# Kernel optimization log

Hardware: AMD Instinct MI355X
Metric: run time of the kernel (lower is better)

## Reference

```python
import jax, jax.numpy as jnp
import numpy as np

EPS = 1e-5  # eps placed on the diagonal via the 'eye' buffer in the torch module


def setup_inputs() -> dict:
    key = jax.random.key(0)
    k1, k2, k3 = jax.random.split(key, 3)
    B, C, H, W = 32, 256, 64, 64
    F = C // 4
    x = jax.random.normal(k1, (B, C, H, W), dtype=jnp.float32)
    # affine mixing weight [4,4,F] (torch inits diag(0.5,1,1,1); we add noise to exercise all paths)
    weight = jnp.eye(4, dtype=jnp.float32)[:, :, None] * jnp.ones((F,), jnp.float32) \
             + 0.1 * jax.random.normal(k2, (4, 4, F), dtype=jnp.float32)
    bias = 0.1 * jax.random.normal(k3, (4, F), dtype=jnp.float32)
    return {"x": x, "weight": weight, "bias": bias}


def reference(x, weight, bias):
    B, C, H, W = x.shape
    F = C // 4
    # split channels into 4 quaternion components: [4, B, F, H, W]
    xq = x.reshape(B, 4, F, H, W).transpose(1, 0, 2, 3, 4)
    # per (component, channel) mean over batch+spatial
    mean = xq.mean(axis=(1, 3, 4))                       # [4, F]
    xc = xq - mean[:, None, :, None, None]               # centered
    N = B * H * W
    # covariance across the 4 quaternion components, per channel: [F, 4, 4]
    v = xc.transpose(2, 0, 1, 3, 4).reshape(F, 4, N)     # [F, 4, N]
    cov = jnp.einsum('fin,fjn->fij', v, v) / N
    # batched 4x4 Cholesky and lower-triangular whitening solve
    L = jnp.linalg.cholesky(cov + EPS * jnp.eye(4, dtype=x.dtype))  # [F, 4, 4]
    z = jax.scipy.linalg.solve_triangular(L, v, lower=True)         # [F, 4, N]
    z = z.reshape(F, 4, B, H, W).transpose(1, 2, 0, 3, 4)           # [4, B, F, H, W]
    # unrolled 4x4 affine mix + bias, per channel
    out = jnp.einsum('ijf,jbfhw->ibfhw', weight, z) + bias[:, None, :, None, None]
    # re-concatenate components along channels -> [B, C, H, W]
    return out.transpose(1, 0, 2, 3, 4).reshape(B, C, H, W)
```

## Files before the change

### kernel.cpp

```cpp
#include <hip/hip_runtime.h>
#include <math.h>

constexpr int B   = 32;
constexpr int C   = 256;
constexpr int F   = 64;
constexpr int HW  = 64 * 64;
constexpr int HW4 = HW / 4;
constexpr int P4  = B * HW4;
constexpr float EPSV = 1e-5f;

constexpr int SBLOCKS = 32;
constexpr int SITER   = P4 / (SBLOCKS * 256);
constexpr int TBLOCKS = P4 / 256;

__global__ __launch_bounds__(256) void stats_kernel(const float* __restrict__ x,
                                                    float* __restrict__ sums) {
    const int f     = blockIdx.x / SBLOCKS;
    const int chunk = blockIdx.x % SBLOCKS;
    const int tid   = threadIdx.x;

    float acc[14];
#pragma unroll
    for (int i = 0; i < 14; ++i) acc[i] = 0.f;

    const float4* xb = reinterpret_cast<const float4*>(x);

#pragma unroll
    for (int it = 0; it < SITER; ++it) {
        const int p   = chunk * (256 * SITER) + it * 256 + tid;
        const int b   = p >> 10;
        const int hw4 = p & (HW4 - 1);
        float4 v[4];
#pragma unroll
        for (int q = 0; q < 4; ++q)
            v[q] = xb[(size_t)(b * C + q * F + f) * HW4 + hw4];
#pragma unroll
        for (int l = 0; l < 4; ++l) {
            float e0 = ((const float*)&v[0])[l];
            float e1 = ((const float*)&v[1])[l];
            float e2 = ((const float*)&v[2])[l];
            float e3 = ((const float*)&v[3])[l];
            acc[0] += e0; acc[1] += e1; acc[2] += e2; acc[3] += e3;
            acc[4]  += e0 * e0; acc[5]  += e0 * e1; acc[6]  += e0 * e2; acc[7]  += e0 * e3;
            acc[8]  += e1 * e1; acc[9]  += e1 * e2; acc[10] += e1 * e3;
            acc[11] += e2 * e2; acc[12] += e2 * e3;
            acc[13] += e3 * e3;
        }
    }

#pragma unroll
    for (int i = 0; i < 14; ++i) {
#pragma unroll
        for (int off = 32; off >= 1; off >>= 1)
            acc[i] += __shfl_down(acc[i], off, 64);
    }

    __shared__ float red[4][14];
    const int wave = tid >> 6;
    const int lane = tid & 63;
    if (lane == 0) {
#pragma unroll
        for (int i = 0; i < 14; ++i) red[wave][i] = acc[i];
    }
    __syncthreads();
    if (tid < 14) {
        float t = red[0][tid] + red[1][tid] + red[2][tid] + red[3][tid];
        atomicAdd(&sums[f * 14 + tid], t);
    }
}

__global__ __launch_bounds__(64) void solve_kernel(const float* __restrict__ sums,
                                                   const float* __restrict__ weight,
                                                   const float* __restrict__ bias,
                                                   float* __restrict__ Mc) {
    const int f = threadIdx.x;
    if (f >= F) return;
    const float invN = 1.0f / (float)(B * HW);

    float m[4];
#pragma unroll
    for (int q = 0; q < 4; ++q) m[q] = sums[f * 14 + q] * invN;

    float cov[4][4];
    {
        int k = 4;
        for (int i = 0; i < 4; ++i)
            for (int j = i; j < 4; ++j) {
                float cij = sums[f * 14 + k] * invN - m[i] * m[j];
                cov[i][j] = cij;
                cov[j][i] = cij;
                ++k;
            }
    }
#pragma unroll
    for (int i = 0; i < 4; ++i) cov[i][i] += EPSV;

    float L[4][4] = {};
    for (int i = 0; i < 4; ++i) {
        for (int j = 0; j <= i; ++j) {
            float s = cov[i][j];
            for (int k = 0; k < j; ++k) s -= L[i][k] * L[j][k];
            if (i == j) L[i][j] = sqrtf(s);
            else        L[i][j] = s / L[j][j];
        }
    }
    float Li[4][4] = {};
    for (int j = 0; j < 4; ++j) {
        Li[j][j] = 1.0f / L[j][j];
        for (int i = j + 1; i < 4; ++i) {
            float s = 0.f;
            for (int k = j; k < i; ++k) s += L[i][k] * Li[k][j];
            Li[i][j] = -s / L[i][i];
        }
    }
    float M[4][4];
    for (int i = 0; i < 4; ++i)
        for (int j = 0; j < 4; ++j) {
            float s = 0.f;
            for (int k = 0; k < 4; ++k)
                s += weight[(i * 4 + k) * F + f] * Li[k][j];
            M[i][j] = s;
        }
    for (int i = 0; i < 4; ++i) {
        float ci = bias[i * F + f];
        for (int j = 0; j < 4; ++j) ci -= M[i][j] * m[j];
#pragma unroll
        for (int j = 0; j < 4; ++j) Mc[f * 20 + i * 4 + j] = M[i][j];
        Mc[f * 20 + 16 + i] = ci;
    }
}

__global__ __launch_bounds__(256) void transform_kernel(const float* __restrict__ x,
                                                        const float* __restrict__ Mc,
                                                        float* __restrict__ out) {
    const int f     = blockIdx.x / TBLOCKS;
    const int chunk = blockIdx.x % TBLOCKS;

    __shared__ float sM[20];
    if (threadIdx.x < 20) sM[threadIdx.x] = Mc[f * 20 + threadIdx.x];
    __syncthreads();

    const int p   = chunk * 256 + threadIdx.x;
    const int b   = p >> 10;
    const int hw4 = p & (HW4 - 1);

    const float4* xb = reinterpret_cast<const float4*>(x);
    float4*       ob = reinterpret_cast<float4*>(out);

    float4 v[4];
#pragma unroll
    for (int q = 0; q < 4; ++q)
        v[q] = xb[(size_t)(b * C + q * F + f) * HW4 + hw4];

#pragma unroll
    for (int i = 0; i < 4; ++i) {
        const float m0 = sM[i * 4 + 0], m1 = sM[i * 4 + 1],
                    m2 = sM[i * 4 + 2], m3 = sM[i * 4 + 3];
        const float ci = sM[16 + i];
        float4 o;
        o.x = ci + m0 * v[0].x + m1 * v[1].x + m2 * v[2].x + m3 * v[3].x;
        o.y = ci + m0 * v[0].y + m1 * v[1].y + m2 * v[2].y + m3 * v[3].y;
        o.z = ci + m0 * v[0].z + m1 * v[1].z + m2 * v[2].z + m3 * v[3].z;
        o.w = ci + m0 * v[0].w + m1 * v[1].w + m2 * v[2].w + m3 * v[3].w;
        ob[(size_t)(b * C + i * F + f) * HW4 + hw4] = o;
    }
}

extern "C" void kernel_launch(void* const* d_in, const int* in_sizes, int n_in,
                              void* d_out, int out_size, void* d_ws, size_t ws_size,
                              hipStream_t stream) {
    const float* x      = (const float*)d_in[0];
    const float* weight = (const float*)d_in[1];
    const float* bias   = (const float*)d_in[2];
    float*       out    = (float*)d_out;

    float* sums = (float*)d_ws;
    float* Mc   = sums + F * 14;

    hipMemsetAsync(sums, 0, F * 14 * sizeof(float), stream);
    stats_kernel<<<F * SBLOCKS, 256, 0, stream>>>(x, sums);
    solve_kernel<<<1, 64, 0, stream>>>(sums, weight, bias, Mc);
    transform_kernel<<<F * TBLOCKS, 256, 0, stream>>>(x, Mc, out);
}
```

Measured before the change: 259.7 us.

## Fuse stats, solve and transform into one cooperative kernel with grid sync

Replaces the memset plus three kernel launches with a single cooperative kernel of 512 blocks. Each block accumulates partial moments for its channel chunk, writes them to workspace, crosses a grid-wide barrier, then reduces its channel's partials, runs the per-channel Cholesky and whitening solve locally, and transforms the same chunk. This removes launch gaps and atomics, and lets the second read of x partly hit in cache. The cost is a grid sync, redundant per-block solves, and reliance on all blocks being co-resident.

Result: slower. 379.4 us (+46.1%).

```diff
diff --git a/kernel.cpp b/kernel.cpp
--- a/kernel.cpp
+++ b/kernel.cpp
@@ -1,45 +1,54 @@
 #include <hip/hip_runtime.h>
+#include <hip/hip_cooperative_groups.h>
 #include <math.h>
 
-constexpr int B   = 32;
-constexpr int C   = 256;
-constexpr int F   = 64;
-constexpr int HW  = 64 * 64;
-constexpr int HW4 = HW / 4;
-constexpr int P4  = B * HW4;
+namespace cg = cooperative_groups;
+
+constexpr int B    = 32;
+constexpr int C    = 256;
+constexpr int F    = 64;
+constexpr int HW4  = 1024;
+constexpr int P4   = B * HW4;
+constexpr int CHUNKS = 8;
+constexpr int NBLK = F * CHUNKS;
+constexpr int PPC  = P4 / CHUNKS;
+constexpr int PPT  = PPC / 256;
 constexpr float EPSV = 1e-5f;
 
-constexpr int SBLOCKS = 32;
-constexpr int SITER   = P4 / (SBLOCKS * 256);
-constexpr int TBLOCKS = P4 / 256;
+__global__ __launch_bounds__(256, 2) void fused_kernel(
+    const float* __restrict__ x,
+    const float* __restrict__ weight,
+    const float* __restrict__ bias,
+    float* __restrict__ out,
+    float* __restrict__ ws)
+{
+    const int f     = blockIdx.x & (F - 1);
+    const int chunk = blockIdx.x >> 6;
+    const int tid   = threadIdx.x;
 
-__global__ __launch_bounds__(256) void stats_kernel(const float* __restrict__ x,
-                                                    float* __restrict__ sums) {
-    const int f     = blockIdx.x / SBLOCKS;
-    const int chunk = blockIdx.x % SBLOCKS;
-    const int tid   = threadIdx.x;
+    const float4* xb = reinterpret_cast<const float4*>(x);
+    const size_t qstride = (size_t)F * HW4;
 
     float acc[14];
 #pragma unroll
     for (int i = 0; i < 14; ++i) acc[i] = 0.f;
 
-    const float4* xb = reinterpret_cast<const float4*>(x);
-
-#pragma unroll
-    for (int it = 0; it < SITER; ++it) {
-        const int p   = chunk * (256 * SITER) + it * 256 + tid;
+#pragma unroll 4
+    for (int it = 0; it < PPT; ++it) {
+        const int p   = chunk * PPC + it * 256 + tid;
         const int b   = p >> 10;
         const int hw4 = p & (HW4 - 1);
-        float4 v[4];
-#pragma unroll
-        for (int q = 0; q < 4; ++q)
-            v[q] = xb[(size_t)(b * C + q * F + f) * HW4 + hw4];
+        const size_t base = ((size_t)b * C + f) * HW4 + hw4;
+        float4 v0 = xb[base];
+        float4 v1 = xb[base + qstride];
+        float4 v2 = xb[base + 2 * qstride];
+        float4 v3 = xb[base + 3 * qstride];
 #pragma unroll
         for (int l = 0; l < 4; ++l) {
-            float e0 = ((const float*)&v[0])[l];
-            float e1 = ((const float*)&v[1])[l];
-            float e2 = ((const float*)&v[2])[l];
-            float e3 = ((const float*)&v[3])[l];
+            const float e0 = ((const float*)&v0)[l];
+            const float e1 = ((const float*)&v1)[l];
+            const float e2 = ((const float*)&v2)[l];
+            const float e3 = ((const float*)&v3)[l];
             acc[0] += e0; acc[1] += e1; acc[2] += e2; acc[3] += e3;
             acc[4]  += e0 * e0; acc[5]  += e0 * e1; acc[6]  += e0 * e2; acc[7]  += e0 * e3;
             acc[8]  += e1 * e1; acc[9]  += e1 * e2; acc[10] += e1 * e3;
@@ -56,6 +65,9 @@
     }
 
     __shared__ float red[4][14];
+    __shared__ float ssum[14];
+    __shared__ float sM[20];
+
     const int wave = tid >> 6;
     const int lane = tid & 63;
     if (lane == 0) {
@@ -64,105 +76,111 @@
     }
     __syncthreads();
     if (tid < 14) {
-        float t = red[0][tid] + red[1][tid] + red[2][tid] + red[3][tid];
-        atomicAdd(&sums[f * 14 + tid], t);
+        ws[(f * CHUNKS + chunk) * 14 + tid] =
+            red[0][tid] + red[1][tid] + red[2][tid] + red[3][tid];
     }
-}
 
-__global__ __launch_bounds__(64) void solve_kernel(const float* __restrict__ sums,
-                                                   const float* __restrict__ weight,
-                                                   const float* __restrict__ bias,
-                                                   float* __restrict__ Mc) {
-    const int f = threadIdx.x;
-    if (f >= F) return;
-    const float invN = 1.0f / (float)(B * HW);
+    __threadfence();
+    cg::this_grid().sync();
 
-    float m[4];
+    if (tid < 14) {
+        float s = 0.f;
 #pragma unroll
-    for (int q = 0; q < 4; ++q) m[q] = sums[f * 14 + q] * invN;
+        for (int c = 0; c < CHUNKS; ++c) s += ws[(f * CHUNKS + c) * 14 + tid];
+        ssum[tid] = s;
+    }
+    __syncthreads();
 
-    float cov[4][4];
-    {
-        int k = 4;
+    if (tid == 0) {
+        const float invN = 1.0f / (float)(B * HW4 * 4);
+        float m[4];
+#pragma unroll
+        for (int q = 0; q < 4; ++q) m[q] = ssum[q] * invN;
+
+        float cov[4][4];
+        {
+            int k = 4;
+            for (int i = 0; i < 4; ++i)
+                for (int j = i; j < 4; ++j) {
+                    float cij = ssum[k] * invN - m[i] * m[j];
+                    cov[i][j] = cij; cov[j][i] = cij; ++k;
+                }
+        }
+#pragma unroll
+        for (int i = 0; i < 4; ++i) cov[i][i] += EPSV;
+
+        float L[4][4] = {};
         for (int i = 0; i < 4; ++i)
-            for (int j = i; j < 4; ++j) {
-                float cij = sums[f * 14 + k] * invN - m[i] * m[j];
-                cov[i][j] = cij;
-                cov[j][i] = cij;
-                ++k;
+            for (int j = 0; j <= i; ++j) {
+                float s = cov[i][j];
+                for (int k = 0; k < j; ++k) s -= L[i][k] * L[j][k];
+                if (i == j) L[i][j] = sqrtf(s);
+                else        L[i][j] = s / L[j][j];
             }
-    }
+
+        float Li[4][4] = {};
+        for (int j = 0; j < 4; ++j) {
+            Li[j][j] = 1.0f / L[j][j];
+            for (int i = j + 1; i < 4; ++i) {
+                float s = 0.f;
+                for (int k = j; k < i; ++k) s += L[i][k] * Li[k][j];
+                Li[i][j] = -s / L[i][i];
+            }
+        }
+
+        float M[4][4];
+        for (int i = 0; i < 4; ++i)
+            for (int j = 0; j < 4; ++j) {
+                float s = 0.f;
+                for (int k = 0; k < 4; ++k)
+                    s += weight[(i * 4 + k) * F + f] * Li[k][j];
+                M[i][j] = s;
+            }
+        for (int i = 0; i < 4; ++i) {
+            float ci = bias[i * F + f];
+            for (int j = 0; j < 4; ++j) ci -= M[i][j] * m[j];
 #pragma unroll
-    for (int i = 0; i < 4; ++i) cov[i][i] += EPSV;
-
-    float L[4][4] = {};
-    for (int i = 0; i < 4; ++i) {
-        for (int j = 0; j <= i; ++j) {
-            float s = cov[i][j];
-            for (int k = 0; k < j; ++k) s -= L[i][k] * L[j][k];
-            if (i == j) L[i][j] = sqrtf(s);
-            else        L[i][j] = s / L[j][j];
+            for (int j = 0; j < 4; ++j) sM[i * 4 + j] = M[i][j];
+            sM[16 + i] = ci;
         }
     }
-    float Li[4][4] = {};
-    for (int j = 0; j < 4; ++j) {
-        Li[j][j] = 1.0f / L[j][j];
-        for (int i = j + 1; i < 4; ++i) {
-            float s = 0.f;
-            for (int k = j; k < i; ++k) s += L[i][k] * Li[k][j];
-            Li[i][j] = -s / L[i][i];
-        }
-    }
-    float M[4][4];
-    for (int i = 0; i < 4; ++i)
-        for (int j = 0; j < 4; ++j) {
-            float s = 0.f;
-            for (int k = 0; k < 4; ++k)
-                s += weight[(i * 4 + k) * F + f] * Li[k][j];
-            M[i][j] = s;
-        }
-    for (int i = 0; i < 4; ++i) {
-        float ci = bias[i * F + f];
-        for (int j = 0; j < 4; ++j) ci -= M[i][j] * m[j];
-#pragma unroll
-        for (int j = 0; j < 4; ++j) Mc[f * 20 + i * 4 + j] = M[i][j];
-        Mc[f * 20 + 16 + i] = ci;
-    }
-}
-
-__global__ __launch_bounds__(256) void transform_kernel(const float* __restrict__ x,
-                                                        const float* __restrict__ Mc,
-                                                        float* __restrict__ out) {
-    const int f     = blockIdx.x / TBLOCKS;
-    const int chunk = blockIdx.x % TBLOCKS;
-
-    __shared__ float sM[20];
-    if (threadIdx.x < 20) sM[threadIdx.x] = Mc[f * 20 + threadIdx.x];
     __syncthreads();
 
-    const int p   = chunk * 256 + threadIdx.x;
-    const int b   = p >> 10;
-    const int hw4 = p & (HW4 - 1);
+    const float m00 = sM[0],  m01 = sM[1],  m02 = sM[2],  m03 = sM[3];
+    const float m10 = sM[4],  m11 = sM[5],  m12 = sM[6],  m13 = sM[7];
+    const float m20 = sM[8],  m21 = sM[9],  m22 = sM[10], m23 = sM[11];
+    const float m30 = sM[12], m31 = sM[13], m32 = sM[14], m33 = sM[15];
+    const float c0 = sM[16], c1 = sM[17], c2 = sM[18], c3 = sM[19];
 
-    const float4* xb = reinterpret_cast<const float4*>(x);
-    float4*       ob = reinterpret_cast<float4*>(out);
+    float4* ob = reinterpret_cast<float4*>(out);
 
-    float4 v[4];
+#pragma unroll 2
+    for (int it = 0; it < PPT; ++it) {
+        const int p   = chunk * PPC + it * 256 + tid;
+        const int b   = p >> 10;
+        const int hw4 = p & (HW4 - 1);
+        const size_t base = ((size_t)b * C + f) * HW4 + hw4;
+        float4 v0 = xb[base];
+        float4 v1 = xb[base + qstride];
+        float4 v2 = xb[base + 2 * qstride];
+        float4 v3 = xb[base + 3 * qstride];
+
+        float4 o0, o1, o2, o3;
 #pragma unroll
-    for (int q = 0; q < 4; ++q)
-        v[q] = xb[(size_t)(b * C + q * F + f) * HW4 + hw4];
-
-#pragma unroll
-    for (int i = 0; i < 4; ++i) {
-        const float m0 = sM[i * 4 + 0], m1 = sM[i * 4 + 1],
-                    m2 = sM[i * 4 + 2], m3 = sM[i * 4 + 3];
-        const float ci = sM[16 + i];
-        float4 o;
-        o.x = ci + m0 * v[0].x + m1 * v[1].x + m2 * v[2].x + m3 * v[3].x;
-        o.y = ci + m0 * v[0].y + m1 * v[1].y + m2 * v[2].y + m3 * v[3].y;
-        o.z = ci + m0 * v[0].z + m1 * v[1].z + m2 * v[2].z + m3 * v[3].z;
-        o.w = ci + m0 * v[0].w + m1 * v[1].w + m2 * v[2].w + m3 * v[3].w;
-        ob[(size_t)(b * C + i * F + f) * HW4 + hw4] = o;
+        for (int l = 0; l < 4; ++l) {
+            const float e0 = ((const float*)&v0)[l];
+            const float e1 = ((const float*)&v1)[l];
+            const float e2 = ((const float*)&v2)[l];
+            const float e3 = ((const float*)&v3)[l];
+            ((float*)&o0)[l] = c0 + m00 * e0 + m01 * e1 + m02 * e2 + m03 * e3;
+            ((float*)&o1)[l] = c1 + m10 * e0 + m11 * e1 + m12 * e2 + m13 * e3;
+            ((float*)&o2)[l] = c2 + m20 * e0 + m21 * e1 + m22 * e2 + m23 * e3;
+            ((float*)&o3)[l] = c3 + m30 * e0 + m31 * e1 + m32 * e2 + m33 * e3;
+        }
+        ob[base]               = o0;
+        ob[base + qstride]     = o1;
+        ob[base + 2 * qstride] = o2;
+        ob[base + 3 * qstride] = o3;
     }
 }
 
@@ -173,12 +191,9 @@
     const float* weight = (const float*)d_in[1];
     const float* bias   = (const float*)d_in[2];
     float*       out    = (float*)d_out;
+    float*       ws     = (float*)d_ws;
 
-    float* sums = (float*)d_ws;
-    float* Mc   = sums + F * 14;
-
-    hipMemsetAsync(sums, 0, F * 14 * sizeof(float), stream);
-    stats_kernel<<<F * SBLOCKS, 256, 0, stream>>>(x, sums);
-    solve_kernel<<<1, 64, 0, stream>>>(sums, weight, bias, Mc);
-    transform_kernel<<<F * TBLOCKS, 256, 0, stream>>>(x, Mc, out);
+    void* args[] = {(void*)&x, (void*)&weight, (void*)&bias, (void*)&out, (void*)&ws};
+    hipLaunchCooperativeKernel((const void*)fused_kernel,
+                               dim3(NBLK), dim3(256), args, 0, stream);
 }
```

## Replace atomics with per-block partials, widen per-thread work, add nontemporal stores

Applied to the files above, without the earlier changes.

The stats kernel now assigns one block per (batch, channel) and writes its partial sums to the workspace instead of atomically adding them. This removes the memset and the atomics, and the solve kernel then reduces the 32 partials per channel. The transform kernel handles two float4 groups per thread and keeps the matrix in registers rather than shared memory, which drops the block sync. Outputs use nontemporal stores to limit cache pollution. Block indexing puts f in the low bits, so neighbouring blocks touch different channels, which could change DRAM locality.

Result: no change. 262.9 us (+1.2%).

```diff
diff --git a/kernel.cpp b/kernel.cpp
--- a/kernel.cpp
+++ b/kernel.cpp
@@ -1,50 +1,54 @@
 #include <hip/hip_runtime.h>
 #include <math.h>
 
-constexpr int B   = 32;
-constexpr int C   = 256;
-constexpr int F   = 64;
-constexpr int HW  = 64 * 64;
-constexpr int HW4 = HW / 4;
-constexpr int P4  = B * HW4;
+constexpr int B    = 32;
+constexpr int C    = 256;
+constexpr int F    = 64;
+constexpr int HW4  = 1024;
 constexpr float EPSV = 1e-5f;
 
-constexpr int SBLOCKS = 32;
-constexpr int SITER   = P4 / (SBLOCKS * 256);
-constexpr int TBLOCKS = P4 / 256;
+typedef float v4f __attribute__((ext_vector_type(4)));
+
 
 __global__ __launch_bounds__(256) void stats_kernel(const float* __restrict__ x,
-                                                    float* __restrict__ sums) {
-    const int f     = blockIdx.x / SBLOCKS;
-    const int chunk = blockIdx.x % SBLOCKS;
-    const int tid   = threadIdx.x;
+                                                    float* __restrict__ ws) {
+    const int f   = blockIdx.x & (F - 1);
+    const int b   = blockIdx.x >> 6;
+    const int tid = threadIdx.x;
+
+    const v4f* xb = reinterpret_cast<const v4f*>(x);
+    const size_t qs    = (size_t)F * HW4;
+    const size_t base0 = ((size_t)b * C + f) * HW4;
 
     float acc[14];
 #pragma unroll
     for (int i = 0; i < 14; ++i) acc[i] = 0.f;
 
-    const float4* xb = reinterpret_cast<const float4*>(x);
-
-#pragma unroll
-    for (int it = 0; it < SITER; ++it) {
-        const int p   = chunk * (256 * SITER) + it * 256 + tid;
-        const int b   = p >> 10;
-        const int hw4 = p & (HW4 - 1);
-        float4 v[4];
-#pragma unroll
-        for (int q = 0; q < 4; ++q)
-            v[q] = xb[(size_t)(b * C + q * F + f) * HW4 + hw4];
-#pragma unroll
-        for (int l = 0; l < 4; ++l) {
-            float e0 = ((const float*)&v[0])[l];
-            float e1 = ((const float*)&v[1])[l];
-            float e2 = ((const float*)&v[2])[l];
-            float e3 = ((const float*)&v[3])[l];
-            acc[0] += e0; acc[1] += e1; acc[2] += e2; acc[3] += e3;
-            acc[4]  += e0 * e0; acc[5]  += e0 * e1; acc[6]  += e0 * e2; acc[7]  += e0 * e3;
-            acc[8]  += e1 * e1; acc[9]  += e1 * e2; acc[10] += e1 * e3;
-            acc[11] += e2 * e2; acc[12] += e2 * e3;
-            acc[13] += e3 * e3;
+#pragma unroll
+    for (int half = 0; half < 2; ++half) {
+        v4f v[2][4];
+#pragma unroll
+        for (int it = 0; it < 2; ++it) {
+            const size_t base = base0 + (half * 2 + it) * 256 + tid;
+            v[it][0] = xb[base];
+            v[it][1] = xb[base + qs];
+            v[it][2] = xb[base + 2 * qs];
+            v[it][3] = xb[base + 3 * qs];
+        }
+#pragma unroll
+        for (int it = 0; it < 2; ++it) {
+#pragma unroll
+            for (int l = 0; l < 4; ++l) {
+                const float e0 = v[it][0][l];
+                const float e1 = v[it][1][l];
+                const float e2 = v[it][2][l];
+                const float e3 = v[it][3][l];
+                acc[0] += e0; acc[1] += e1; acc[2] += e2; acc[3] += e3;
+                acc[4]  += e0 * e0; acc[5]  += e0 * e1; acc[6]  += e0 * e2; acc[7]  += e0 * e3;
+                acc[8]  += e1 * e1; acc[9]  += e1 * e2; acc[10] += e1 * e3;
+                acc[11] += e2 * e2; acc[12] += e2 * e3;
+                acc[13] += e3 * e3;
+            }
         }
     }
 
@@ -64,62 +68,70 @@
     }
     __syncthreads();
     if (tid < 14) {
-        float t = red[0][tid] + red[1][tid] + red[2][tid] + red[3][tid];
-        atomicAdd(&sums[f * 14 + tid], t);
-    }
-}
-
-__global__ __launch_bounds__(64) void solve_kernel(const float* __restrict__ sums,
+        ws[(size_t)blockIdx.x * 14 + tid] =
+            red[0][tid] + red[1][tid] + red[2][tid] + red[3][tid];
+    }
+}
+
+__global__ __launch_bounds__(64) void solve_kernel(const float* __restrict__ ws,
                                                    const float* __restrict__ weight,
                                                    const float* __restrict__ bias,
                                                    float* __restrict__ Mc) {
     const int f = threadIdx.x;
     if (f >= F) return;
-    const float invN = 1.0f / (float)(B * HW);
-
+
+    float s[14];
+#pragma unroll
+    for (int i = 0; i < 14; ++i) s[i] = 0.f;
+    for (int b = 0; b < B; ++b) {
+        const float* p = ws + ((size_t)(b * F + f)) * 14;
+#pragma unroll
+        for (int i = 0; i < 14; ++i) s[i] += p[i];
+    }
+
+    const float invN = 1.0f / (float)(B * HW4 * 4);
     float m[4];
 #pragma unroll
-    for (int q = 0; q < 4; ++q) m[q] = sums[f * 14 + q] * invN;
+    for (int q = 0; q < 4; ++q) m[q] = s[q] * invN;
 
     float cov[4][4];
     {
         int k = 4;
         for (int i = 0; i < 4; ++i)
             for (int j = i; j < 4; ++j) {
-                float cij = sums[f * 14 + k] * invN - m[i] * m[j];
-                cov[i][j] = cij;
-                cov[j][i] = cij;
-                ++k;
+                float cij = s[k] * invN - m[i] * m[j];
+                cov[i][j] = cij; cov[j][i] = cij; ++k;
             }
     }
 #pragma unroll
     for (int i = 0; i < 4; ++i) cov[i][i] += EPSV;
 
     float L[4][4] = {};
-    for (int i = 0; i < 4; ++i) {
+    for (int i = 0; i < 4; ++i)
         for (int j = 0; j <= i; ++j) {
-            float s = cov[i][j];
-            for (int k = 0; k < j; ++k) s -= L[i][k] * L[j][k];
-            if (i == j) L[i][j] = sqrtf(s);
-            else        L[i][j] = s / L[j][j];
-        }
-    }
+            float t = cov[i][j];
+            for (int k = 0; k < j; ++k) t -= L[i][k] * L[j][k];
+            if (i == j) L[i][j] = sqrtf(t);
+            else        L[i][j] = t / L[j][j];
+        }
+
     float Li[4][4] = {};
     for (int j = 0; j < 4; ++j) {
         Li[j][j] = 1.0f / L[j][j];
         for (int i = j + 1; i < 4; ++i) {
-            float s = 0.f;
-            for (int k = j; k < i; ++k) s += L[i][k] * Li[k][j];
-            Li[i][j] = -s / L[i][i];
-        }
-    }
+            float t = 0.f;
+            for (int k = j; k < i; ++k) t += L[i][k] * Li[k][j];
+            Li[i][j] = -t / L[i][i];
+        }
+    }
+
     float M[4][4];
     for (int i = 0; i < 4; ++i)
         for (int j = 0; j < 4; ++j) {
-            float s = 0.f;
+            float t = 0.f;
             for (int k = 0; k < 4; ++k)
-                s += weight[(i * 4 + k) * F + f] * Li[k][j];
-            M[i][j] = s;
+                t += weight[(i * 4 + k) * F + f] * Li[k][j];
+            M[i][j] = t;
         }
     for (int i = 0; i < 4; ++i) {
         float ci = bias[i * F + f];
@@ -133,36 +145,54 @@
 __global__ __launch_bounds__(256) void transform_kernel(const float* __restrict__ x,
                                                         const float* __restrict__ Mc,
                                                         float* __restrict__ out) {
-    const int f     = blockIdx.x / TBLOCKS;
-    const int chunk = blockIdx.x % TBLOCKS;
-
-    __shared__ float sM[20];
-    if (threadIdx.x < 20) sM[threadIdx.x] = Mc[f * 20 + threadIdx.x];
-    __syncthreads();
-
-    const int p   = chunk * 256 + threadIdx.x;
-    const int b   = p >> 10;
-    const int hw4 = p & (HW4 - 1);
-
-    const float4* xb = reinterpret_cast<const float4*>(x);
-    float4*       ob = reinterpret_cast<float4*>(out);
-
-    float4 v[4];
-#pragma unroll
-    for (int q = 0; q < 4; ++q)
-        v[q] = xb[(size_t)(b * C + q * F + f) * HW4 + hw4];
-
-#pragma unroll
-    for (int i = 0; i < 4; ++i) {
-        const float m0 = sM[i * 4 + 0], m1 = sM[i * 4 + 1],
-                    m2 = sM[i * 4 + 2], m3 = sM[i * 4 + 3];
-        const float ci = sM[16 + i];
-        float4 o;
-        o.x = ci + m0 * v[0].x + m1 * v[1].x + m2 * v[2].x + m3 * v[3].x;
-        o.y = ci + m0 * v[0].y + m1 * v[1].y + m2 * v[2].y + m3 * v[3].y;
-        o.z = ci + m0 * v[0].z + m1 * v[1].z + m2 * v[2].z + m3 * v[3].z;
-        o.w = ci + m0 * v[0].w + m1 * v[1].w + m2 * v[2].w + m3 * v[3].w;
-        ob[(size_t)(b * C + i * F + f) * HW4 + hw4] = o;
+    const int f   = blockIdx.x & (F - 1);
+    const int c   = blockIdx.x >> 6;
+    const int tid = threadIdx.x;
+
+    const float* Mf = Mc + f * 20;
+    const float m00 = Mf[0],  m01 = Mf[1],  m02 = Mf[2],  m03 = Mf[3];
+    const float m10 = Mf[4],  m11 = Mf[5],  m12 = Mf[6],  m13 = Mf[7];
+    const float m20 = Mf[8],  m21 = Mf[9],  m22 = Mf[10], m23 = Mf[11];
+    const float m30 = Mf[12], m31 = Mf[13], m32 = Mf[14], m33 = Mf[15];
+    const float c0 = Mf[16], c1 = Mf[17], c2 = Mf[18], c3 = Mf[19];
+
+    const int b    = c >> 1;
+    const int hw0  = (c & 1) * 512 + tid;
+
+    const v4f* xb = reinterpret_cast<const v4f*>(x);
+    v4f*       ob = reinterpret_cast<v4f*>(out);
+    const size_t qs    = (size_t)F * HW4;
+    const size_t base0 = ((size_t)b * C + f) * HW4 + hw0;
+
+    v4f v[2][4];
+#pragma unroll
+    for (int it = 0; it < 2; ++it) {
+        const size_t base = base0 + it * 256;
+        v[it][0] = xb[base];
+        v[it][1] = xb[base + qs];
+        v[it][2] = xb[base + 2 * qs];
+        v[it][3] = xb[base + 3 * qs];
+    }
+
+#pragma unroll
+    for (int it = 0; it < 2; ++it) {
+        const size_t base = base0 + it * 256;
+        v4f o0, o1, o2, o3;
+#pragma unroll
+        for (int l = 0; l < 4; ++l) {
+            const float e0 = v[it][0][l];
+            const float e1 = v[it][1][l];
+            const float e2 = v[it][2][l];
+            const float e3 = v[it][3][l];
+            o0[l] = c0 + m00 * e0 + m01 * e1 + m02 * e2 + m03 * e3;
+            o1[l] = c1 + m10 * e0 + m11 * e1 + m12 * e2 + m13 * e3;
+            o2[l] = c2 + m20 * e0 + m21 * e1 + m22 * e2 + m23 * e3;
+            o3[l] = c3 + m30 * e0 + m31 * e1 + m32 * e2 + m33 * e3;
+        }
+        __builtin_nontemporal_store(o0, &ob[base]);
+        __builtin_nontemporal_store(o1, &ob[base + qs]);
+        __builtin_nontemporal_store(o2, &ob[base + 2 * qs]);
+        __builtin_nontemporal_store(o3, &ob[base + 3 * qs]);
     }
 }
 
@@ -174,11 +204,10 @@
     const float* bias   = (const float*)d_in[2];
     float*       out    = (float*)d_out;
 
-    float* sums = (float*)d_ws;
-    float* Mc   = sums + F * 14;
-
-    hipMemsetAsync(sums, 0, F * 14 * sizeof(float), stream);
-    stats_kernel<<<F * SBLOCKS, 256, 0, stream>>>(x, sums);
-    solve_kernel<<<1, 64, 0, stream>>>(sums, weight, bias, Mc);
-    transform_kernel<<<F * TBLOCKS, 256, 0, stream>>>(x, Mc, out);
-}
+    float* ws = (float*)d_ws;
+    float* Mc = ws + 2048 * 14;
+
+    stats_kernel<<<dim3(F * B), dim3(256), 0, stream>>>(x, ws);
+    solve_kernel<<<dim3(1), dim3(64), 0, stream>>>(ws, weight, bias, Mc);
+    transform_kernel<<<dim3(F * 64), dim3(256), 0, stream>>>(x, Mc, out);
+}
```
